# Kernel tuning notes

Hardware: AMD Instinct MI355X
Metric: run time of the kernel (lower is better)

Reference implementation:

```python
import jax, jax.numpy as jnp
import numpy as np


def setup_inputs() -> dict:
    key = jax.random.key(0)
    x = jax.random.normal(key, (32, 1, 1024, 2048), dtype=jnp.float32)
    return {"x": x}


def reference(x):
    # Cumulative max along dim 2 (the original Python loop does an in-place
    # prefix-max over rows of channel 0). Since C == 1, applying it to the
    # whole channel axis is equivalent; for C > 1 only channel 0 would change.
    scanned = jax.lax.cummax(x[:, 0:1, :, :], axis=2)  # [B,1,H,W]
    if x.shape[1] == 1:
        return scanned
    return jnp.concatenate([scanned, x[:, 1:, :, :]], axis=1)
```

## Files before the change

### kernel.cpp

```cpp
#include <hip/hip_runtime.h>


#define B 32
#define H 1024
#define W 2048

__global__ __launch_bounds__(64) void cummax_h_kernel(
    const float* __restrict__ x, float* __restrict__ out) {
  const int p  = blockIdx.x * 64 + threadIdx.x;
  const int b  = p >> 10;
  const int wp = p & 1023;

  const size_t base = ((size_t)b << 20) + (size_t)wp;
  const float2* __restrict__ px = reinterpret_cast<const float2*>(x) + base;
  float2* __restrict__ po       = reinterpret_cast<float2*>(out) + base;

  float2 m;
  m.x = -__builtin_inff();
  m.y = -__builtin_inff();

#pragma unroll 16
  for (int h = 0; h < H; ++h) {
    float2 v = px[(size_t)h * (W / 2)];
    m.x = fmaxf(m.x, v.x);
    m.y = fmaxf(m.y, v.y);
    po[(size_t)h * (W / 2)] = m;
  }
}

extern "C" void kernel_launch(void* const* d_in, const int* in_sizes, int n_in,
                              void* d_out, int out_size, void* d_ws, size_t ws_size,
                              hipStream_t stream) {
  const float* x = (const float*)d_in[0];
  float* out = (float*)d_out;

  const int n_pairs = B * W / 2;
  const int block = 64;
  const int grid = n_pairs / block;
  cummax_h_kernel<<<grid, block, 0, stream>>>(x, out);
}
```

Baseline: 452.8 us.

## Process one column per thread with double-buffered chunked prefetch

Switches from one float2 column-pair per thread in 64-thread blocks to one float column per thread in 256-thread blocks, which doubles the thread count to 65536. Each thread software-pipelines its scan: it loads the next 16 rows into a register buffer while computing and storing the previous 16, so more loads are in flight to hide memory latency. The trade-offs are scalar instead of 64-bit accesses and higher register use from the two buffers.

```diff
diff --git a/kernel.cpp b/kernel.cpp
--- a/kernel.cpp
+++ b/kernel.cpp
@@ -4,27 +4,62 @@
 #define B 32
 #define H 1024
 #define W 2048
+#define CH 16
+#define NCHUNK (H / CH)
 
-__global__ __launch_bounds__(64) void cummax_h_kernel(
+__global__ __launch_bounds__(256) void cummax_h_kernel(
     const float* __restrict__ x, float* __restrict__ out) {
-  const int p  = blockIdx.x * 64 + threadIdx.x;
-  const int b  = p >> 10;
-  const int wp = p & 1023;
+  const int col = blockIdx.x * 256 + threadIdx.x;
+  const int b = col >> 11;
+  const int w = col & (W - 1);
 
-  const size_t base = ((size_t)b << 20) + (size_t)wp;
-  const float2* __restrict__ px = reinterpret_cast<const float2*>(x) + base;
-  float2* __restrict__ po       = reinterpret_cast<float2*>(out) + base;
+  const size_t base = (size_t)b * (H * W) + (size_t)w;
+  const float* __restrict__ px = x + base;
+  float* __restrict__ po = out + base;
 
-  float2 m;
-  m.x = -__builtin_inff();
-  m.y = -__builtin_inff();
+  float bufA[CH], bufB[CH];
+  float m = -__builtin_inff();
 
-#pragma unroll 16
-  for (int h = 0; h < H; ++h) {
-    float2 v = px[(size_t)h * (W / 2)];
-    m.x = fmaxf(m.x, v.x);
-    m.y = fmaxf(m.y, v.y);
-    po[(size_t)h * (W / 2)] = m;
+#pragma unroll
+  for (int i = 0; i < CH; ++i) bufA[i] = px[(size_t)i * W];
+  px += (size_t)CH * W;
+
+  for (int c = 0; c < NCHUNK - 2; c += 2) {
+#pragma unroll
+    for (int i = 0; i < CH; ++i) bufB[i] = px[(size_t)i * W];
+    px += (size_t)CH * W;
+
+#pragma unroll
+    for (int i = 0; i < CH; ++i) {
+      m = fmaxf(m, bufA[i]);
+      po[(size_t)i * W] = m;
+    }
+    po += (size_t)CH * W;
+
+#pragma unroll
+    for (int i = 0; i < CH; ++i) bufA[i] = px[(size_t)i * W];
+    px += (size_t)CH * W;
+
+#pragma unroll
+    for (int i = 0; i < CH; ++i) {
+      m = fmaxf(m, bufB[i]);
+      po[(size_t)i * W] = m;
+    }
+    po += (size_t)CH * W;
+  }
+
+#pragma unroll
+  for (int i = 0; i < CH; ++i) bufB[i] = px[(size_t)i * W];
+#pragma unroll
+  for (int i = 0; i < CH; ++i) {
+    m = fmaxf(m, bufA[i]);
+    po[(size_t)i * W] = m;
+  }
+  po += (size_t)CH * W;
+#pragma unroll
+  for (int i = 0; i < CH; ++i) {
+    m = fmaxf(m, bufB[i]);
+    po[(size_t)i * W] = m;
   }
 }
 
@@ -34,8 +69,8 @@
   const float* x = (const float*)d_in[0];
   float* out = (float*)d_out;
 
-  const int n_pairs = B * W / 2;
-  const int block = 64;
-  const int grid = n_pairs / block;
+  const int n_cols = B * W;
+  const int block = 256;
+  const int grid = n_cols / block;
   cummax_h_kernel<<<grid, block, 0, stream>>>(x, out);
 }
```

New measurement: 427.3 us. -5.6%, faster.
